# Kernel optimization log

Hardware: AMD Instinct MI355X
Metric: run time of the kernel (lower is better)

## Reference

```python
import jax, jax.numpy as jnp
import numpy as np

TAU = 0.1          # contrastive_temperature
EPS = 0.05         # property_epsilon
L_LOCAL_G, L_GLOBAL, L_SC_G, L_LOCAL_SC, G_PROP = 1.0, 0.8, 1.0, 0.8, 0.5
B = 4096
D = 256
NUM_PROPS = 4
N_ATOMS = 131072
N_MOTIFS = 32768


def setup_inputs() -> dict:
    key = jax.random.key(0)
    ks = jax.random.split(key, 10)
    return {
        "emb_g_mole": jax.random.normal(ks[0], (B, D), jnp.float32),
        "emb_g_frag": jax.random.normal(ks[1], (N_ATOMS, D), jnp.float32),
        "emb_sc_mole": jax.random.normal(ks[2], (B, D), jnp.float32),
        "emb_sc_shape": jax.random.normal(ks[3], (N_MOTIFS, D), jnp.float32),
        "emb_motif": jax.random.normal(ks[4], (N_MOTIFS, D), jnp.float32),
        "emb_shape": jax.random.normal(ks[5], (N_MOTIFS, D), jnp.float32),
        # scaled so duplicate rows are the only pairs within EPS (realistic sparse mask)
        "prop_pred": jax.random.normal(ks[6], (B, NUM_PROPS), jnp.float32) * 0.05,
        "prop_target": jax.random.normal(ks[7], (B, NUM_PROPS), jnp.float32) * 0.05,
        "batch_g": jax.random.randint(ks[8], (N_ATOMS,), 0, B, jnp.int32),
        "batch_sc": jax.random.randint(ks[9], (N_MOTIFS,), 0, B, jnp.int32),
    }


def _contrastive(emb, props):
    # SupervisedContrastiveLoss: normalized cosine logits, mask from sqrt(cdist) < eps
    n = emb.shape[0]
    e = emb / jnp.maximum(jnp.linalg.norm(emb, axis=1, keepdims=True), 1e-12)
    logits = jnp.matmul(e, e.T) / TAU                       # [n, n]
    log_probs = jax.nn.log_softmax(logits, axis=1)
    sq = jnp.sum(props * props, axis=1)
    d2 = jnp.maximum(sq[:, None] + sq[None, :] - 2.0 * jnp.matmul(props, props.T), 0.0)
    dd = jnp.sqrt(jnp.sqrt(d2)) + 1e-8                      # cdist(...).sqrt() + 1e-8
    mask = (dd < EPS) & (~jnp.eye(n, dtype=bool))           # fill_diagonal_(0)
    cnt = jnp.sum(mask, axis=1)
    row_loss = -jnp.sum(jnp.where(mask, log_probs, 0.0), axis=1) / jnp.maximum(cnt, 1)
    valid = cnt > 0
    nvalid = jnp.sum(valid)
    loss = jnp.sum(jnp.where(valid, row_loss, 0.0)) / jnp.maximum(nvalid, 1)
    return jnp.where(nvalid > 0, loss, 0.0)


def _frag_alignment(emb_g_frag, emb_motif, batch_g, batch_sc):
    ones_g = jnp.ones((emb_g_frag.shape[0],), emb_g_frag.dtype)
    ones_s = jnp.ones((emb_motif.shape[0],), emb_motif.dtype)
    cnt_g = jax.ops.segment_sum(ones_g, batch_g, num_segments=B)
    cnt_s = jax.ops.segment_sum(ones_s, batch_sc, num_segments=B)
    mean_g = jax.ops.segment_sum(emb_g_frag, batch_g, num_segments=B) / jnp.maximum(cnt_g, 1.0)[:, None]
    mean_s = jax.ops.segment_sum(emb_motif, batch_sc, num_segments=B) / jnp.maximum(cnt_s, 1.0)[:, None]
    norms = jnp.linalg.norm(mean_g - mean_s, axis=1)
    valid = (cnt_g > 0) & (cnt_s > 0)
    batch_size = batch_g.max().astype(emb_g_frag.dtype) + 1.0
    return jnp.sum(jnp.where(valid, norms, 0.0)) / batch_size


def reference(emb_g_mole, emb_g_frag, emb_sc_mole, emb_sc_shape, emb_motif,
              emb_shape, prop_pred, prop_target, batch_g, batch_sc):
    l_local_g = _frag_alignment(emb_g_frag, emb_motif, batch_g, batch_sc)
    combined_emb = jnp.concatenate([emb_g_mole, emb_sc_mole], axis=0)    # [2B, d]
    combined_props = jnp.concatenate([prop_pred, prop_pred], axis=0)      # [2B, p]
    l_contr = _contrastive(combined_emb, combined_props)
    l_global = l_contr          # same inputs in both calls -> identical value
    l_local_sc = l_contr
    l_sc_g = jnp.mean(jnp.linalg.norm(emb_sc_shape - emb_shape, axis=1))  # AlignmentLoss mean
    l_prop = jnp.mean((prop_pred - prop_target) ** 2)                     # MSELoss
    l_hes = (L_LOCAL_G * l_local_g + L_GLOBAL * l_global + L_SC_G * l_sc_g
             + L_LOCAL_SC * l_local_sc + G_PROP * l_prop)
    # stacked: [l_hes, l_local_g, l_global, l_sc_g, l_local_sc, l_prop]
    return jnp.stack([l_hes, l_local_g, l_global, l_sc_g, l_local_sc, l_prop])
```

## Files before the change

### kernel.cpp

```cpp
#include <hip/hip_runtime.h>
#include <hip/hip_bf16.h>
#include <stdint.h>

typedef unsigned short u16;
typedef float f32x4 __attribute__((ext_vector_type(4)));
typedef short s16x8 __attribute__((ext_vector_type(8)));
typedef u16   u16x8 __attribute__((ext_vector_type(8)));
typedef u16   u16x4 __attribute__((ext_vector_type(4)));
typedef uint32_t u32x4 __attribute__((ext_vector_type(4)));

#define B_      4096
#define D_      256
#define NA_     131072
#define NM_     32768
#define N2_     8192
#define THR4    6.2499950e-6f
#define K2E     14.426950408889634f

#define OFF_CNT_G   0u
#define OFF_CNT_S   16384u
#define OFF_CUR_G   32768u
#define OFF_CUR_S   49152u
#define OFF_NB      65536u
#define OFF_SCAL    81920u
#define ZERO_BYTES  98304u
#define OFF_T       98304u
#define OFF_C       131072u
#define OFF_S       163840u
#define OFF_PLIST   196608u
#define OFF_OFFS_G  720896u
#define OFF_OFFS_S  737280u
#define OFF_SORT_G  753664u
#define OFF_SORT_S  1277952u
#define OFF_SP      753664u
#define OFF_E       4947968u
#define WS_NEED     9142272u

__device__ inline float wave_sum(float v) {
#pragma unroll
  for (int m = 1; m < 64; m <<= 1) v += __shfl_xor(v, m, 64);
  return v;
}
__device__ inline int wave_sum_i(int v) {
#pragma unroll
  for (int m = 1; m < 64; m <<= 1) v += __shfl_xor(v, m, 64);
  return v;
}
__device__ inline u16 f2bf(float f) {
  uint32_t u = __float_as_uint(f);
  uint32_t r = (u + 0x7FFFu + ((u >> 16) & 1u)) >> 16;
  return (u16)r;
}
__device__ inline float bf2f(u16 v) { return __uint_as_float(((uint32_t)v) << 16); }

__device__ inline void gload16(const u16* __restrict__ g, u16* l) {
  __builtin_amdgcn_global_load_lds(
      (const __attribute__((address_space(1))) uint32_t*)g,
      (__attribute__((address_space(3))) uint32_t*)l, 16, 0, 0);
}

__global__ void k_zero(u32x4* __restrict__ p) {
  u32x4 z = {0u, 0u, 0u, 0u};
  p[blockIdx.x * 256 + threadIdx.x] = z;
}

__global__ void k_count(const int* __restrict__ bg, const int* __restrict__ bs,
                        int* cntg, int* cnts, int* bmax) {
  int i = blockIdx.x * 256 + threadIdx.x;
  int b = -1;
  if (i < NA_) { b = bg[i]; atomicAdd(&cntg[b], 1); }
  if (i < NM_) { atomicAdd(&cnts[bs[i]], 1); }
  int m = b;
#pragma unroll
  for (int k = 1; k < 64; k <<= 1) m = max(m, __shfl_xor(m, k, 64));
  if ((threadIdx.x & 63) == 0 && m >= 0) atomicMax(bmax, m);
}

__global__ void k_scan(const int* __restrict__ cntg, const int* __restrict__ cnts,
                       int* offsg, int* offss, int* curg, int* curs) {
  const int* cnt = blockIdx.x == 0 ? cntg : cnts;
  int* offs = blockIdx.x == 0 ? offsg : offss;
  int* cur  = blockIdx.x == 0 ? curg  : curs;
  __shared__ int ls[256];
  int t = threadIdx.x;
  int v[16]; int s = 0;
#pragma unroll
  for (int k = 0; k < 16; k++) { v[k] = cnt[t * 16 + k]; s += v[k]; }
  ls[t] = s;
  __syncthreads();
  for (int off = 1; off < 256; off <<= 1) {
    int add = (t >= off) ? ls[t - off] : 0;
    __syncthreads();
    ls[t] += add;
    __syncthreads();
  }
  int pre = t ? ls[t - 1] : 0;
#pragma unroll
  for (int k = 0; k < 16; k++) { offs[t * 16 + k] = pre; cur[t * 16 + k] = pre; pre += v[k]; }
}

__global__ void k_scatter(const int* __restrict__ bg, const int* __restrict__ bs,
                          int* curg, int* curs, int* sortg, int* sorts) {
  int i = blockIdx.x * 256 + threadIdx.x;
  if (i < NA_) { int b = bg[i]; sortg[atomicAdd(&curg[b], 1)] = i; }
  if (i < NM_) { int b = bs[i]; sorts[atomicAdd(&curs[b], 1)] = i; }
}

__device__ inline void wave_row_sum(const float* __restrict__ src,
                                    const int* __restrict__ sorted,
                                    int off, int cnt, int lane, f32x4* accs) {
  f32x4 a0 = {0.f,0.f,0.f,0.f}, a1 = a0, a2 = a0, a3 = a0;
  f32x4 a4 = a0, a5 = a0, a6 = a0, a7 = a0;
  for (int base = 0; base < cnt; base += 64) {
    int n = min(cnt - base, 64);
    int idx = (lane < n) ? sorted[off + base + lane] : 0;
    int k = 0;
    for (; k + 7 < n; k += 8) {
      int i0 = __shfl(idx, k,     64), i1 = __shfl(idx, k + 1, 64);
      int i2 = __shfl(idx, k + 2, 64), i3 = __shfl(idx, k + 3, 64);
      int i4 = __shfl(idx, k + 4, 64), i5 = __shfl(idx, k + 5, 64);
      int i6 = __shfl(idx, k + 6, 64), i7 = __shfl(idx, k + 7, 64);
      a0 += *(const f32x4*)(src + (size_t)i0 * D_ + lane * 4);
      a1 += *(const f32x4*)(src + (size_t)i1 * D_ + lane * 4);
      a2 += *(const f32x4*)(src + (size_t)i2 * D_ + lane * 4);
      a3 += *(const f32x4*)(src + (size_t)i3 * D_ + lane * 4);
      a4 += *(const f32x4*)(src + (size_t)i4 * D_ + lane * 4);
      a5 += *(const f32x4*)(src + (size_t)i5 * D_ + lane * 4);
      a6 += *(const f32x4*)(src + (size_t)i6 * D_ + lane * 4);
      a7 += *(const f32x4*)(src + (size_t)i7 * D_ + lane * 4);
    }
    for (; k < n; k++) {
      int i0 = __shfl(idx, k, 64);
      a0 += *(const f32x4*)(src + (size_t)i0 * D_ + lane * 4);
    }
  }
  *accs = ((a0 + a1) + (a2 + a3)) + ((a4 + a5) + (a6 + a7));
}

__global__ __launch_bounds__(256) void k_fuse1(
    const float* __restrict__ fg, const float* __restrict__ fm,
    const int* __restrict__ cntg, const int* __restrict__ cnts,
    const int* __restrict__ offsg, const int* __restrict__ offss,
    const int* __restrict__ sortg, const int* __restrict__ sorts,
    const float* __restrict__ scs, const float* __restrict__ shp,
    const float* __restrict__ gm, const float* __restrict__ scm,
    const float* __restrict__ pp,
    u16* __restrict__ E, int* __restrict__ nb, int* __restrict__ plist,
    float* __restrict__ scal) {
  int t = threadIdx.x, w = t >> 6, lane = t & 63;
  int blk = blockIdx.x;
  __shared__ float sr4[4];

  if (blk < 1024) {
    int b = blk * 4 + w;
    int cg = cntg[b], cs = cnts[b];
    int og = offsg[b], os = offss[b];
    f32x4 sg, ss;
    wave_row_sum(fg, sortg, og, cg, lane, &sg);
    wave_row_sum(fm, sorts, os, cs, lane, &ss);
    float ig = 1.f / fmaxf((float)cg, 1.f);
    float is = 1.f / fmaxf((float)cs, 1.f);
    float dx = sg.x * ig - ss.x * is, dy = sg.y * ig - ss.y * is;
    float dz = sg.z * ig - ss.z * is, dw = sg.w * ig - ss.w * is;
    float v = wave_sum(dx * dx + dy * dy + dz * dz + dw * dw);
    if (lane == 0) sr4[w] = (cg > 0 && cs > 0) ? sqrtf(v) : 0.f;
    __syncthreads();
    if (t == 0) {
      float s = sr4[0] + sr4[1] + sr4[2] + sr4[3];
      if (s != 0.f) atomicAdd(&scal[0], s);
    }
  } else if (blk < 3072) {
    int wg = (blk - 1024) * 4 + w;
    float acc = 0.f;
    for (int r = wg; r < NM_; r += 8192) {
      f32x4 va = *(const f32x4*)(scs + (size_t)r * D_ + lane * 4);
      f32x4 vb = *(const f32x4*)(shp + (size_t)r * D_ + lane * 4);
      float dx = va.x - vb.x, dy = va.y - vb.y, dz = va.z - vb.z, dw = va.w - vb.w;
      float ss = wave_sum(dx * dx + dy * dy + dz * dz + dw * dw);
      if (lane == 0) acc += sqrtf(ss);
    }
    if (lane == 0) sr4[w] = acc;
    __syncthreads();
    if (t == 0) atomicAdd(&scal[1], sr4[0] + sr4[1] + sr4[2] + sr4[3]);
  } else if (blk < 5120) {
    int r = (blk - 3072) * 4 + w;
    const float* src = (r < B_) ? gm + (size_t)r * D_ : scm + (size_t)(r - B_) * D_;
    f32x4 v = *(const f32x4*)(src + lane * 4);
    float ss = v.x * v.x + v.y * v.y + v.z * v.z + v.w * v.w;
    ss = wave_sum(ss);
    float inv = 1.f / fmaxf(sqrtf(ss), 1e-12f);
    u16x4 o;
    o.x = f2bf(v.x * inv); o.y = f2bf(v.y * inv);
    o.z = f2bf(v.z * inv); o.w = f2bf(v.w * inv);
    *(u16x4*)(E + (size_t)r * D_ + lane * 4) = o;
  } else {
    int a = blk - 5120;
    f32x4 pa = *(const f32x4*)(pp + (size_t)a * 4);
    for (int b = t; b < B_; b += 256) {
      f32x4 pb = *(const f32x4*)(pp + (size_t)b * 4);
      float dx = pa.x - pb.x, dy = pa.y - pb.y, dz = pa.z - pb.z, dw = pa.w - pb.w;
      float d2 = dx * dx + dy * dy + dz * dz + dw * dw;
      if (d2 < THR4) {
        int pos = atomicAdd(&nb[a], 1);
        if (pos < 32) plist[a * 32 + pos] = b;
      }
    }
  }
}

__global__ __launch_bounds__(256) void k_gemm(const u16* __restrict__ E,
                                              float* __restrict__ SP) {
  __shared__ __align__(16) u16 As[128 * 64];
  __shared__ __align__(16) u16 Bs[128 * 64];

  int t = blockIdx.x;
  int bi = (int)((129.0f - sqrtf(129.0f * 129.0f - 8.0f * (float)t)) * 0.5f);
  while ((bi + 1) * (129 - (bi + 1)) / 2 <= t) bi++;
  while (bi * (129 - bi) / 2 > t) bi--;
  int bj = bi + (t - bi * (129 - bi) / 2);

  int row0 = bi * 128, col0 = bj * 128;
  int tid = threadIdx.x, lane = tid & 63, wid = tid >> 6;
  int wr = wid >> 1, wc = wid & 1;

  int rsub = lane >> 3;
  int csw  = (((lane & 7) ^ rsub) << 4) >> 1;

  f32x4 acc[4][4];
#pragma unroll
  for (int mi = 0; mi < 4; mi++)
#pragma unroll
    for (int ni = 0; ni < 4; ni++) {
      f32x4 z = {0.f, 0.f, 0.f, 0.f};
      acc[mi][ni] = z;
    }

  for (int kc = 0; kc < 4; ++kc) {
    __syncthreads();
#pragma unroll
    for (int it = 0; it < 4; it++) {
      int s = wid * 4 + it;
      int r = s * 8 + rsub;
      gload16(E + (size_t)(row0 + r) * D_ + kc * 64 + csw, As + s * 512);
      gload16(E + (size_t)(col0 + r) * D_ + kc * 64 + csw, Bs + s * 512);
    }
    __syncthreads();
#pragma unroll
    for (int kk = 0; kk < 2; ++kk) {
      s16x8 af[4], bfr[4];
#pragma unroll
      for (int mi = 0; mi < 4; mi++) {
        int rA = wr * 64 + mi * 16 + (lane & 15);
        int cbf = kk * 64 + (lane >> 4) * 16;
        int addr = rA * 128 + (cbf ^ ((rA & 7) << 4));
        af[mi] = *(const s16x8*)((const char*)As + addr);
      }
#pragma unroll
      for (int ni = 0; ni < 4; ni++) {
        int rB = wc * 64 + ni * 16 + (lane & 15);
        int cbf = kk * 64 + (lane >> 4) * 16;
        int addr = rB * 128 + (cbf ^ ((rB & 7) << 4));
        bfr[ni] = *(const s16x8*)((const char*)Bs + addr);
      }
#pragma unroll
      for (int mi = 0; mi < 4; mi++)
#pragma unroll
        for (int ni = 0; ni < 4; ni++)
          acc[mi][ni] = __builtin_amdgcn_mfma_f32_16x16x32_bf16(af[mi], bfr[ni], acc[mi][ni], 0, 0, 0);
    }
  }

  int g = lane >> 4, cl = lane & 15;
  int sliceR = bj * 2 + wc;
  float colsum[4] = {0.f, 0.f, 0.f, 0.f};
#pragma unroll
  for (int mi = 0; mi < 4; mi++) {
#pragma unroll
    for (int reg = 0; reg < 4; ++reg) {
      int gi = row0 + wr * 64 + mi * 16 + g * 4 + reg;
      float vs = 0.f;
#pragma unroll
      for (int ni = 0; ni < 4; ni++) {
        float e = exp2f(acc[mi][ni][reg] * K2E - K2E);
        vs += e;
        colsum[ni] += e;
      }
#pragma unroll
      for (int m = 1; m < 16; m <<= 1) vs += __shfl_xor(vs, m, 64);
      if (cl == 0) SP[(size_t)sliceR * N2_ + gi] = vs;
    }
  }
  if (bi != bj) {
    int sliceC = bi * 2 + wr;
#pragma unroll
    for (int ni = 0; ni < 4; ni++) {
      float cs = colsum[ni];
      cs += __shfl_xor(cs, 16, 64);
      cs += __shfl_xor(cs, 32, 64);
      if (g == 0) SP[(size_t)sliceC * N2_ + col0 + wc * 64 + ni * 16 + cl] = cs;
    }
  }
}

__global__ __launch_bounds__(256) void k_fuse2(
    const float* __restrict__ SP, float* __restrict__ S,
    const u16* __restrict__ E, const int* __restrict__ nb,
    const int* __restrict__ plist, float* __restrict__ T, int* __restrict__ C) {
  int blk = blockIdx.x;
  if (blk < 32) {
    int gi = blk * 256 + threadIdx.x;
    float s = 0.f;
    for (int k = 0; k < 128; k++) s += SP[(size_t)k * N2_ + gi];
    S[gi] = s;
  } else {
    int w = threadIdx.x >> 6, lane = threadIdx.x & 63;
    int i = (blk - 32) * 4 + w;
    int a = i & (B_ - 1);
    int n = min(nb[a], 32);
    u16x4 vi = *(const u16x4*)(E + (size_t)i * D_ + lane * 4);
    float ex = bf2f(vi.x), ey = bf2f(vi.y), ez = bf2f(vi.z), ew = bf2f(vi.w);
    float acc = -(ex * ex + ey * ey + ez * ez + ew * ew);
    for (int k = 0; k < n; k++) {
      int b = plist[a * 32 + k];
      u16x4 v1 = *(const u16x4*)(E + (size_t)b * D_ + lane * 4);
      u16x4 v2 = *(const u16x4*)(E + (size_t)(b + B_) * D_ + lane * 4);
      acc += ex * bf2f(v1.x) + ey * bf2f(v1.y) + ez * bf2f(v1.z) + ew * bf2f(v1.w);
      acc += ex * bf2f(v2.x) + ey * bf2f(v2.y) + ez * bf2f(v2.z) + ew * bf2f(v2.w);
    }
    acc = wave_sum(acc);
    if (lane == 0) { T[i] = 10.0f * acc; C[i] = 2 * n - 1; }
  }
}

__global__ void k_final(const float* __restrict__ S, const float* __restrict__ T,
                        const int* __restrict__ C, const float* __restrict__ scal,
                        const float* __restrict__ pp, const float* __restrict__ pt,
                        float* __restrict__ out) {
  float sp = 0.f;
  for (int i = threadIdx.x; i < B_ * 4; i += 256) {
    float d = pp[i] - pt[i];
    sp += d * d;
  }
  float rls = 0.f; int nv = 0;
  for (int i = threadIdx.x; i < N2_; i += 256) {
    int ci = C[i];
    if (ci > 0) { rls += (10.0f + logf(S[i])) - T[i] / (float)ci; nv++; }
  }
  rls = wave_sum(rls);
  sp  = wave_sum(sp);
  nv  = wave_sum_i(nv);
  __shared__ float r1[4], r3[4]; __shared__ int r2[4];
  int lane = threadIdx.x & 63, w = threadIdx.x >> 6;
  if (lane == 0) { r1[w] = rls; r2[w] = nv; r3[w] = sp; }
  __syncthreads();
  if (threadIdx.x == 0) {
    float rtot = r1[0] + r1[1] + r1[2] + r1[3];
    int nvt = r2[0] + r2[1] + r2[2] + r2[3];
    float sptot = r3[0] + r3[1] + r3[2] + r3[3];
    float l_contr = nvt > 0 ? rtot / (float)nvt : 0.f;
    int bmax = ((const int*)scal)[3];
    float bs = (float)bmax + 1.0f;
    float l_local_g = scal[0] / bs;
    float l_sc = scal[1] / (float)NM_;
    float l_prop = sptot / (float)(B_ * 4);
    float l_hes = 1.0f * l_local_g + 0.8f * l_contr + 1.0f * l_sc + 0.8f * l_contr + 0.5f * l_prop;
    out[0] = l_hes; out[1] = l_local_g; out[2] = l_contr;
    out[3] = l_sc;  out[4] = l_contr;   out[5] = l_prop;
  }
}

extern "C" void kernel_launch(void* const* d_in, const int* in_sizes, int n_in,
                              void* d_out, int out_size, void* d_ws, size_t ws_size,
                              hipStream_t stream) {
  if (ws_size < WS_NEED) return;
  const float* gm  = (const float*)d_in[0];
  const float* fg  = (const float*)d_in[1];
  const float* scm = (const float*)d_in[2];
  const float* scs = (const float*)d_in[3];
  const float* mot = (const float*)d_in[4];
  const float* shp = (const float*)d_in[5];
  const float* pp  = (const float*)d_in[6];
  const float* pt  = (const float*)d_in[7];
  const int* bg = (const int*)d_in[8];
  const int* bs = (const int*)d_in[9];
  float* out = (float*)d_out;
  char* ws = (char*)d_ws;

  int* cntg  = (int*)(ws + OFF_CNT_G);
  int* cnts  = (int*)(ws + OFF_CNT_S);
  int* curg  = (int*)(ws + OFF_CUR_G);
  int* curs  = (int*)(ws + OFF_CUR_S);
  int* nb    = (int*)(ws + OFF_NB);
  float* scal = (float*)(ws + OFF_SCAL);
  float* T   = (float*)(ws + OFF_T);
  int* C     = (int*)(ws + OFF_C);
  float* S   = (float*)(ws + OFF_S);
  int* plist = (int*)(ws + OFF_PLIST);
  int* offsg = (int*)(ws + OFF_OFFS_G);
  int* offss = (int*)(ws + OFF_OFFS_S);
  int* sortg = (int*)(ws + OFF_SORT_G);
  int* sorts = (int*)(ws + OFF_SORT_S);
  float* SP  = (float*)(ws + OFF_SP);
  u16* E     = (u16*)(ws + OFF_E);

  k_zero<<<24, 256, 0, stream>>>((u32x4*)ws);
  k_count<<<512, 256, 0, stream>>>(bg, bs, cntg, cnts, (int*)scal + 3);
  k_scan<<<2, 256, 0, stream>>>(cntg, cnts, offsg, offss, curg, curs);
  k_scatter<<<512, 256, 0, stream>>>(bg, bs, curg, curs, sortg, sorts);
  k_fuse1<<<9216, 256, 0, stream>>>(fg, mot, cntg, cnts, offsg, offss, sortg, sorts,
                                    scs, shp, gm, scm, pp, E, nb, plist, scal);
  k_gemm<<<2080, 256, 0, stream>>>(E, SP);
  k_fuse2<<<2080, 256, 0, stream>>>(SP, S, E, nb, plist, T, C);
  k_final<<<1, 256, 0, stream>>>(S, T, C, scal, pp, pt, out);
}
```

Baseline: 215.4 us.

## Regroup stages into two fused kernels and accumulate softmax sums atomically

Merges the scatter, normalization, shape-alignment and neighbor-list work into one kernel. The GEMM/softmax-sum, fragment alignment and positive-pair dot products are merged into a second kernel, which removes two launches and the serial dependency chain between them. The per-slice partial-sum buffer and its reduction pass are replaced by float atomicAdd into a zeroed S array, which also shrinks the workspace. In exchange the summation order becomes nondeterministic, there is atomic contention on S, and heterogeneous blocks (LDS-heavy GEMM tiles mixed with gather blocks) share one launch, which may affect occupancy.

```diff
diff --git a/kernel.cpp b/kernel.cpp
--- a/kernel.cpp
+++ b/kernel.cpp
@@ -23,18 +23,17 @@
 #define OFF_CUR_S   49152u
 #define OFF_NB      65536u
 #define OFF_SCAL    81920u
-#define ZERO_BYTES  98304u
-#define OFF_T       98304u
-#define OFF_C       131072u
-#define OFF_S       163840u
+#define OFF_S       98304u
+#define ZERO_BYTES  131072u
+#define OFF_T       131072u
+#define OFF_C       163840u
 #define OFF_PLIST   196608u
 #define OFF_OFFS_G  720896u
 #define OFF_OFFS_S  737280u
 #define OFF_SORT_G  753664u
 #define OFF_SORT_S  1277952u
-#define OFF_SP      753664u
-#define OFF_E       4947968u
-#define WS_NEED     9142272u
+#define OFF_E       1409024u
+#define WS_NEED     5603328u
 
 __device__ inline float wave_sum(float v) {
 #pragma unroll
@@ -97,13 +96,6 @@
   int pre = t ? ls[t - 1] : 0;
 #pragma unroll
   for (int k = 0; k < 16; k++) { offs[t * 16 + k] = pre; cur[t * 16 + k] = pre; pre += v[k]; }
-}
-
-__global__ void k_scatter(const int* __restrict__ bg, const int* __restrict__ bs,
-                          int* curg, int* curs, int* sortg, int* sorts) {
-  int i = blockIdx.x * 256 + threadIdx.x;
-  if (i < NA_) { int b = bg[i]; sortg[atomicAdd(&curg[b], 1)] = i; }
-  if (i < NM_) { int b = bs[i]; sorts[atomicAdd(&curs[b], 1)] = i; }
 }
 
 __device__ inline void wave_row_sum(const float* __restrict__ src,
@@ -137,22 +129,78 @@
   *accs = ((a0 + a1) + (a2 + a3)) + ((a4 + a5) + (a6 + a7));
 }
 
-__global__ __launch_bounds__(256) void k_fuse1(
-    const float* __restrict__ fg, const float* __restrict__ fm,
-    const int* __restrict__ cntg, const int* __restrict__ cnts,
-    const int* __restrict__ offsg, const int* __restrict__ offss,
-    const int* __restrict__ sortg, const int* __restrict__ sorts,
+__global__ __launch_bounds__(256) void k_fuseA(
+    const int* __restrict__ bg, const int* __restrict__ bs,
+    int* __restrict__ curg, int* __restrict__ curs,
+    int* __restrict__ sortg, int* __restrict__ sorts,
+    const float* __restrict__ gm, const float* __restrict__ scm,
     const float* __restrict__ scs, const float* __restrict__ shp,
-    const float* __restrict__ gm, const float* __restrict__ scm,
     const float* __restrict__ pp,
     u16* __restrict__ E, int* __restrict__ nb, int* __restrict__ plist,
     float* __restrict__ scal) {
   int t = threadIdx.x, w = t >> 6, lane = t & 63;
   int blk = blockIdx.x;
-  __shared__ float sr4[4];
+
+  if (blk < 4096) {
+    int a = blk;
+    f32x4 pa = *(const f32x4*)(pp + (size_t)a * 4);
+    for (int b = t; b < B_; b += 256) {
+      f32x4 pb = *(const f32x4*)(pp + (size_t)b * 4);
+      float dx = pa.x - pb.x, dy = pa.y - pb.y, dz = pa.z - pb.z, dw = pa.w - pb.w;
+      float d2 = dx * dx + dy * dy + dz * dz + dw * dw;
+      if (d2 < THR4) {
+        int pos = atomicAdd(&nb[a], 1);
+        if (pos < 32) plist[a * 32 + pos] = b;
+      }
+    }
+  } else if (blk < 4608) {
+    int i = (blk - 4096) * 256 + t;
+    if (i < NA_) { int b = bg[i]; sortg[atomicAdd(&curg[b], 1)] = i; }
+    if (i < NM_) { int b = bs[i]; sorts[atomicAdd(&curs[b], 1)] = i; }
+  } else if (blk < 6656) {
+    int r = (blk - 4608) * 4 + w;
+    const float* src = (r < B_) ? gm + (size_t)r * D_ : scm + (size_t)(r - B_) * D_;
+    f32x4 v = *(const f32x4*)(src + lane * 4);
+    float ss = v.x * v.x + v.y * v.y + v.z * v.z + v.w * v.w;
+    ss = wave_sum(ss);
+    float inv = 1.f / fmaxf(sqrtf(ss), 1e-12f);
+    u16x4 o;
+    o.x = f2bf(v.x * inv); o.y = f2bf(v.y * inv);
+    o.z = f2bf(v.z * inv); o.w = f2bf(v.w * inv);
+    *(u16x4*)(E + (size_t)r * D_ + lane * 4) = o;
+  } else {
+    int wg = (blk - 6656) * 4 + w;
+    float acc = 0.f;
+    for (int r = wg; r < NM_; r += 8192) {
+      f32x4 va = *(const f32x4*)(scs + (size_t)r * D_ + lane * 4);
+      f32x4 vb = *(const f32x4*)(shp + (size_t)r * D_ + lane * 4);
+      float dx = va.x - vb.x, dy = va.y - vb.y, dz = va.z - vb.z, dw = va.w - vb.w;
+      float ss = wave_sum(dx * dx + dy * dy + dz * dz + dw * dw);
+      if (lane == 0) acc += sqrtf(ss);
+    }
+    __shared__ float sr4[4];
+    if (lane == 0) sr4[w] = acc;
+    __syncthreads();
+    if (t == 0) atomicAdd(&scal[1], sr4[0] + sr4[1] + sr4[2] + sr4[3]);
+  }
+}
+
+__global__ __launch_bounds__(256) void k_fuseB(
+    const u16* __restrict__ E,
+    const float* __restrict__ fg, const float* __restrict__ fm,
+    const int* __restrict__ cntg, const int* __restrict__ cnts,
+    const int* __restrict__ offsg, const int* __restrict__ offss,
+    const int* __restrict__ sortg, const int* __restrict__ sorts,
+    const int* __restrict__ nb, const int* __restrict__ plist,
+    float* __restrict__ S, float* __restrict__ T, int* __restrict__ C,
+    float* __restrict__ scal) {
+  __shared__ __align__(16) u16 As[128 * 64];
+  __shared__ __align__(16) u16 Bs[128 * 64];
+  int blk = blockIdx.x;
+  int tid = threadIdx.x, lane = tid & 63, wid = tid >> 6;
 
   if (blk < 1024) {
-    int b = blk * 4 + w;
+    int b = blk * 4 + wid;
     int cg = cntg[b], cs = cnts[b];
     int og = offsg[b], os = offss[b];
     f32x4 sg, ss;
@@ -163,158 +211,18 @@
     float dx = sg.x * ig - ss.x * is, dy = sg.y * ig - ss.y * is;
     float dz = sg.z * ig - ss.z * is, dw = sg.w * ig - ss.w * is;
     float v = wave_sum(dx * dx + dy * dy + dz * dz + dw * dw);
-    if (lane == 0) sr4[w] = (cg > 0 && cs > 0) ? sqrtf(v) : 0.f;
-    __syncthreads();
-    if (t == 0) {
-      float s = sr4[0] + sr4[1] + sr4[2] + sr4[3];
+    __shared__ float r2[4];
+    if (lane == 0) r2[wid] = (cg > 0 && cs > 0) ? sqrtf(v) : 0.f;
+    __syncthreads();
+    if (tid == 0) {
+      float s = r2[0] + r2[1] + r2[2] + r2[3];
       if (s != 0.f) atomicAdd(&scal[0], s);
     }
-  } else if (blk < 3072) {
-    int wg = (blk - 1024) * 4 + w;
-    float acc = 0.f;
-    for (int r = wg; r < NM_; r += 8192) {
-      f32x4 va = *(const f32x4*)(scs + (size_t)r * D_ + lane * 4);
-      f32x4 vb = *(const f32x4*)(shp + (size_t)r * D_ + lane * 4);
-      float dx = va.x - vb.x, dy = va.y - vb.y, dz = va.z - vb.z, dw = va.w - vb.w;
-      float ss = wave_sum(dx * dx + dy * dy + dz * dz + dw * dw);
-      if (lane == 0) acc += sqrtf(ss);
-    }
-    if (lane == 0) sr4[w] = acc;
-    __syncthreads();
-    if (t == 0) atomicAdd(&scal[1], sr4[0] + sr4[1] + sr4[2] + sr4[3]);
-  } else if (blk < 5120) {
-    int r = (blk - 3072) * 4 + w;
-    const float* src = (r < B_) ? gm + (size_t)r * D_ : scm + (size_t)(r - B_) * D_;
-    f32x4 v = *(const f32x4*)(src + lane * 4);
-    float ss = v.x * v.x + v.y * v.y + v.z * v.z + v.w * v.w;
-    ss = wave_sum(ss);
-    float inv = 1.f / fmaxf(sqrtf(ss), 1e-12f);
-    u16x4 o;
-    o.x = f2bf(v.x * inv); o.y = f2bf(v.y * inv);
-    o.z = f2bf(v.z * inv); o.w = f2bf(v.w * inv);
-    *(u16x4*)(E + (size_t)r * D_ + lane * 4) = o;
-  } else {
-    int a = blk - 5120;
-    f32x4 pa = *(const f32x4*)(pp + (size_t)a * 4);
-    for (int b = t; b < B_; b += 256) {
-      f32x4 pb = *(const f32x4*)(pp + (size_t)b * 4);
-      float dx = pa.x - pb.x, dy = pa.y - pb.y, dz = pa.z - pb.z, dw = pa.w - pb.w;
-      float d2 = dx * dx + dy * dy + dz * dz + dw * dw;
-      if (d2 < THR4) {
-        int pos = atomicAdd(&nb[a], 1);
-        if (pos < 32) plist[a * 32 + pos] = b;
-      }
-    }
-  }
-}
-
-__global__ __launch_bounds__(256) void k_gemm(const u16* __restrict__ E,
-                                              float* __restrict__ SP) {
-  __shared__ __align__(16) u16 As[128 * 64];
-  __shared__ __align__(16) u16 Bs[128 * 64];
-
-  int t = blockIdx.x;
-  int bi = (int)((129.0f - sqrtf(129.0f * 129.0f - 8.0f * (float)t)) * 0.5f);
-  while ((bi + 1) * (129 - (bi + 1)) / 2 <= t) bi++;
-  while (bi * (129 - bi) / 2 > t) bi--;
-  int bj = bi + (t - bi * (129 - bi) / 2);
-
-  int row0 = bi * 128, col0 = bj * 128;
-  int tid = threadIdx.x, lane = tid & 63, wid = tid >> 6;
-  int wr = wid >> 1, wc = wid & 1;
-
-  int rsub = lane >> 3;
-  int csw  = (((lane & 7) ^ rsub) << 4) >> 1;
-
-  f32x4 acc[4][4];
-#pragma unroll
-  for (int mi = 0; mi < 4; mi++)
-#pragma unroll
-    for (int ni = 0; ni < 4; ni++) {
-      f32x4 z = {0.f, 0.f, 0.f, 0.f};
-      acc[mi][ni] = z;
-    }
-
-  for (int kc = 0; kc < 4; ++kc) {
-    __syncthreads();
-#pragma unroll
-    for (int it = 0; it < 4; it++) {
-      int s = wid * 4 + it;
-      int r = s * 8 + rsub;
-      gload16(E + (size_t)(row0 + r) * D_ + kc * 64 + csw, As + s * 512);
-      gload16(E + (size_t)(col0 + r) * D_ + kc * 64 + csw, Bs + s * 512);
-    }
-    __syncthreads();
-#pragma unroll
-    for (int kk = 0; kk < 2; ++kk) {
-      s16x8 af[4], bfr[4];
-#pragma unroll
-      for (int mi = 0; mi < 4; mi++) {
-        int rA = wr * 64 + mi * 16 + (lane & 15);
-        int cbf = kk * 64 + (lane >> 4) * 16;
-        int addr = rA * 128 + (cbf ^ ((rA & 7) << 4));
-        af[mi] = *(const s16x8*)((const char*)As + addr);
-      }
-#pragma unroll
-      for (int ni = 0; ni < 4; ni++) {
-        int rB = wc * 64 + ni * 16 + (lane & 15);
-        int cbf = kk * 64 + (lane >> 4) * 16;
-        int addr = rB * 128 + (cbf ^ ((rB & 7) << 4));
-        bfr[ni] = *(const s16x8*)((const char*)Bs + addr);
-      }
-#pragma unroll
-      for (int mi = 0; mi < 4; mi++)
-#pragma unroll
-        for (int ni = 0; ni < 4; ni++)
-          acc[mi][ni] = __builtin_amdgcn_mfma_f32_16x16x32_bf16(af[mi], bfr[ni], acc[mi][ni], 0, 0, 0);
-    }
-  }
-
-  int g = lane >> 4, cl = lane & 15;
-  int sliceR = bj * 2 + wc;
-  float colsum[4] = {0.f, 0.f, 0.f, 0.f};
-#pragma unroll
-  for (int mi = 0; mi < 4; mi++) {
-#pragma unroll
-    for (int reg = 0; reg < 4; ++reg) {
-      int gi = row0 + wr * 64 + mi * 16 + g * 4 + reg;
-      float vs = 0.f;
-#pragma unroll
-      for (int ni = 0; ni < 4; ni++) {
-        float e = exp2f(acc[mi][ni][reg] * K2E - K2E);
-        vs += e;
-        colsum[ni] += e;
-      }
-#pragma unroll
-      for (int m = 1; m < 16; m <<= 1) vs += __shfl_xor(vs, m, 64);
-      if (cl == 0) SP[(size_t)sliceR * N2_ + gi] = vs;
-    }
-  }
-  if (bi != bj) {
-    int sliceC = bi * 2 + wr;
-#pragma unroll
-    for (int ni = 0; ni < 4; ni++) {
-      float cs = colsum[ni];
-      cs += __shfl_xor(cs, 16, 64);
-      cs += __shfl_xor(cs, 32, 64);
-      if (g == 0) SP[(size_t)sliceC * N2_ + col0 + wc * 64 + ni * 16 + cl] = cs;
-    }
-  }
-}
-
-__global__ __launch_bounds__(256) void k_fuse2(
-    const float* __restrict__ SP, float* __restrict__ S,
-    const u16* __restrict__ E, const int* __restrict__ nb,
-    const int* __restrict__ plist, float* __restrict__ T, int* __restrict__ C) {
-  int blk = blockIdx.x;
-  if (blk < 32) {
-    int gi = blk * 256 + threadIdx.x;
-    float s = 0.f;
-    for (int k = 0; k < 128; k++) s += SP[(size_t)k * N2_ + gi];
-    S[gi] = s;
-  } else {
-    int w = threadIdx.x >> 6, lane = threadIdx.x & 63;
-    int i = (blk - 32) * 4 + w;
+    return;
+  }
+
+  if (blk >= 3104) {
+    int i = (blk - 3104) * 4 + wid;
     int a = i & (B_ - 1);
     int n = min(nb[a], 32);
     u16x4 vi = *(const u16x4*)(E + (size_t)i * D_ + lane * 4);
@@ -329,6 +237,92 @@
     }
     acc = wave_sum(acc);
     if (lane == 0) { T[i] = 10.0f * acc; C[i] = 2 * n - 1; }
+    return;
+  }
+
+  int t = blk - 1024;
+  int bi = (int)((129.0f - sqrtf(129.0f * 129.0f - 8.0f * (float)t)) * 0.5f);
+  while ((bi + 1) * (129 - (bi + 1)) / 2 <= t) bi++;
+  while (bi * (129 - bi) / 2 > t) bi--;
+  int bj = bi + (t - bi * (129 - bi) / 2);
+
+  int row0 = bi * 128, col0 = bj * 128;
+  int wr = wid >> 1, wc = wid & 1;
+
+  int rsub = lane >> 3;
+  int csw  = (((lane & 7) ^ rsub) << 4) >> 1;
+
+  f32x4 acc[4][4];
+#pragma unroll
+  for (int mi = 0; mi < 4; mi++)
+#pragma unroll
+    for (int ni = 0; ni < 4; ni++) {
+      f32x4 z = {0.f, 0.f, 0.f, 0.f};
+      acc[mi][ni] = z;
+    }
+
+  for (int kc = 0; kc < 4; ++kc) {
+    __syncthreads();
+#pragma unroll
+    for (int it = 0; it < 4; it++) {
+      int s = wid * 4 + it;
+      int r = s * 8 + rsub;
+      gload16(E + (size_t)(row0 + r) * D_ + kc * 64 + csw, As + s * 512);
+      gload16(E + (size_t)(col0 + r) * D_ + kc * 64 + csw, Bs + s * 512);
+    }
+    __syncthreads();
+#pragma unroll
+    for (int kk = 0; kk < 2; ++kk) {
+      s16x8 af[4], bfr[4];
+#pragma unroll
+      for (int mi = 0; mi < 4; mi++) {
+        int rA = wr * 64 + mi * 16 + (lane & 15);
+        int cbf = kk * 64 + (lane >> 4) * 16;
+        int addr = rA * 128 + (cbf ^ ((rA & 7) << 4));
+        af[mi] = *(const s16x8*)((const char*)As + addr);
+      }
+#pragma unroll
+      for (int ni = 0; ni < 4; ni++) {
+        int rB = wc * 64 + ni * 16 + (lane & 15);
+        int cbf = kk * 64 + (lane >> 4) * 16;
+        int addr = rB * 128 + (cbf ^ ((rB & 7) << 4));
+        bfr[ni] = *(const s16x8*)((const char*)Bs + addr);
+      }
+#pragma unroll
+      for (int mi = 0; mi < 4; mi++)
+#pragma unroll
+        for (int ni = 0; ni < 4; ni++)
+          acc[mi][ni] = __builtin_amdgcn_mfma_f32_16x16x32_bf16(af[mi], bfr[ni], acc[mi][ni], 0, 0, 0);
+    }
+  }
+
+  int g = lane >> 4, cl = lane & 15;
+  float colsum[4] = {0.f, 0.f, 0.f, 0.f};
+#pragma unroll
+  for (int mi = 0; mi < 4; mi++) {
+#pragma unroll
+    for (int reg = 0; reg < 4; ++reg) {
+      int gi = row0 + wr * 64 + mi * 16 + g * 4 + reg;
+      float vs = 0.f;
+#pragma unroll
+      for (int ni = 0; ni < 4; ni++) {
+        float e = exp2f(acc[mi][ni][reg] * K2E - K2E);
+        vs += e;
+        colsum[ni] += e;
+      }
+#pragma unroll
+      for (int m = 1; m < 16; m <<= 1) vs += __shfl_xor(vs, m, 64);
+      if (cl == 0) atomicAdd(&S[gi], vs);
+    }
+  }
+  if (bi != bj) {
+#pragma unroll
+    for (int ni = 0; ni < 4; ni++) {
+      float cs = colsum[ni];
+      cs += __shfl_xor(cs, 16, 64);
+      cs += __shfl_xor(cs, 32, 64);
+      if (g == 0) atomicAdd(&S[col0 + wc * 64 + ni * 16 + cl], cs);
+    }
   }
 }
 
@@ -392,24 +386,22 @@
   int* curs  = (int*)(ws + OFF_CUR_S);
   int* nb    = (int*)(ws + OFF_NB);
   float* scal = (float*)(ws + OFF_SCAL);
+  float* S   = (float*)(ws + OFF_S);
   float* T   = (float*)(ws + OFF_T);
   int* C     = (int*)(ws + OFF_C);
-  float* S   = (float*)(ws + OFF_S);
   int* plist = (int*)(ws + OFF_PLIST);
   int* offsg = (int*)(ws + OFF_OFFS_G);
   int* offss = (int*)(ws + OFF_OFFS_S);
   int* sortg = (int*)(ws + OFF_SORT_G);
   int* sorts = (int*)(ws + OFF_SORT_S);
-  float* SP  = (float*)(ws + OFF_SP);
   u16* E     = (u16*)(ws + OFF_E);
 
-  k_zero<<<24, 256, 0, stream>>>((u32x4*)ws);
+  k_zero<<<32, 256, 0, stream>>>((u32x4*)ws);
   k_count<<<512, 256, 0, stream>>>(bg, bs, cntg, cnts, (int*)scal + 3);
   k_scan<<<2, 256, 0, stream>>>(cntg, cnts, offsg, offss, curg, curs);
-  k_scatter<<<512, 256, 0, stream>>>(bg, bs, curg, curs, sortg, sorts);
-  k_fuse1<<<9216, 256, 0, stream>>>(fg, mot, cntg, cnts, offsg, offss, sortg, sorts,
-                                    scs, shp, gm, scm, pp, E, nb, plist, scal);
-  k_gemm<<<2080, 256, 0, stream>>>(E, SP);
-  k_fuse2<<<2080, 256, 0, stream>>>(SP, S, E, nb, plist, T, C);
+  k_fuseA<<<8704, 256, 0, stream>>>(bg, bs, curg, curs, sortg, sorts,
+                                    gm, scm, scs, shp, pp, E, nb, plist, scal);
+  k_fuseB<<<5152, 256, 0, stream>>>(E, fg, mot, cntg, cnts, offsg, offss,
+                                    sortg, sorts, nb, plist, S, T, C, scal);
   k_final<<<1, 256, 0, stream>>>(S, T, C, scal, pp, pt, out);
 }
```

New measurement: 213.4 us. No clear change (-0.9%).
